# Kernel tuning notes

Measured on AMD Instinct MI355X. Metric: run time of the kernel, lower is better.

The kernel has to match this reference:

```python
import jax, jax.numpy as jnp
import numpy as np

DIM = 2048
NH = 16
Q_LORA = 1536
KV_LORA = 512
NOPE = 128
ROPE = 64
VDIM = 128
QK = NOPE + ROPE  # 192
B, S = 2, 2048
EPS = 1.1920929e-07  # torch.finfo(float32).eps (nn.RMSNorm default)


def linear(x, w, b):
    return jnp.einsum('...i,oi->...o', x, w) + b


def rmsnorm(x, w):
    ms = jnp.mean(x * x, axis=-1, keepdims=True)
    return x * jax.lax.rsqrt(ms + EPS) * w


def rope(x, cos, sin):
    # x: [B,S,H,d] interleaved pairs; cos/sin: [S, d//2]
    x = x.reshape(*x.shape[:-1], -1, 2)
    x0, x1 = x[..., 0], x[..., 1]
    c = cos[None, :, None, :]
    s = sin[None, :, None, :]
    y0 = x0 * c - x1 * s
    y1 = x0 * s + x1 * c
    return jnp.stack([y0, y1], axis=-1).reshape(*x.shape[:-2], -1)


def setup_inputs() -> dict:
    key = jax.random.key(0)
    ks = jax.random.split(key, 12)
    sd = 0.02
    x = jax.random.normal(ks[0], (B, S, DIM), dtype=jnp.float32)
    freqs = jax.random.normal(ks[1], (S, ROPE // 2), dtype=jnp.float32)
    causal_mask = jnp.where(jnp.triu(jnp.ones((S, S), bool), k=1), -1e9, 0.0).astype(jnp.float32)
    inp = dict(x=x, freqs=freqs, causal_mask=causal_mask)
    inp['Wq_down_w'] = sd * jax.random.normal(ks[2], (Q_LORA, DIM), dtype=jnp.float32)
    inp['Wq_down_b'] = jnp.zeros((Q_LORA,), jnp.float32)
    inp['q_norm_w'] = jnp.ones((Q_LORA,), jnp.float32)
    inp['Wq_up_w'] = sd * jax.random.normal(ks[3], (NH * QK, Q_LORA), dtype=jnp.float32)
    inp['Wq_up_b'] = jnp.zeros((NH * QK,), jnp.float32)
    inp['Wkv_down_w'] = sd * jax.random.normal(ks[4], (KV_LORA + ROPE, DIM), dtype=jnp.float32)
    inp['Wkv_down_b'] = jnp.zeros((KV_LORA + ROPE,), jnp.float32)
    inp['kv_norm_w'] = jnp.ones((KV_LORA,), jnp.float32)
    inp['Wkv_up_w'] = sd * jax.random.normal(ks[5], (NH * (NOPE + VDIM), KV_LORA), dtype=jnp.float32)
    inp['Wkv_up_b'] = jnp.zeros((NH * (NOPE + VDIM),), jnp.float32)
    inp['Wo_w'] = sd * jax.random.normal(ks[6], (DIM, NH * VDIM), dtype=jnp.float32)
    inp['Wo_b'] = jnp.zeros((DIM,), jnp.float32)
    return inp


def reference(x, freqs, causal_mask, Wq_down_w, Wq_down_b, q_norm_w, Wq_up_w, Wq_up_b,
              Wkv_down_w, Wkv_down_b, kv_norm_w, Wkv_up_w, Wkv_up_b, Wo_w, Wo_b):
    cos, sin = jnp.cos(freqs), jnp.sin(freqs)
    scale = QK ** -0.5
    # Q path: low-rank down, RMSNorm, up
    q_lat = rmsnorm(linear(x, Wq_down_w, Wq_down_b), q_norm_w)
    Q = linear(q_lat, Wq_up_w, Wq_up_b).reshape(B, S, NH, QK)
    Q_nope, Q_rope = Q[..., :NOPE], Q[..., NOPE:]
    Q_rope = rope(Q_rope, cos, sin)
    Q = jnp.concatenate([Q_nope, Q_rope], axis=-1)  # [B,S,H,QK]
    # KV path: shared latent + decoupled rope key
    kv_kr = linear(x, Wkv_down_w, Wkv_down_b)
    kv_lat, K_rope = kv_kr[..., :KV_LORA], kv_kr[..., KV_LORA:]
    kv_lat = rmsnorm(kv_lat, kv_norm_w)
    K_rope = rope(K_rope[:, :, None, :], cos, sin)  # [B,S,1,ROPE]
    kv = linear(kv_lat, Wkv_up_w, Wkv_up_b).reshape(B, S, NH, NOPE + VDIM)
    K_nope, V = kv[..., :NOPE], kv[..., NOPE:]
    K = jnp.concatenate([K_nope, jnp.broadcast_to(K_rope, (B, S, NH, ROPE))], axis=-1)
    # attention
    scores = jnp.einsum('bqhd,bkhd->bhqk', Q, K) * scale + causal_mask[None, None]
    attn = jax.nn.softmax(scores, axis=-1)
    out = jnp.einsum('bhqk,bkhd->bqhd', attn, V).reshape(B, S, NH * VDIM)
    return linear(out, Wo_w, Wo_b)
```

## Files before the change

kernel.cpp:

```cpp
#include <hip/hip_runtime.h>
#include <hip/hip_bf16.h>

#define DIMD 2048
#define NHD 16
#define QLORA 1536
#define KVLORA 512
#define QKD 192
#define BBD 2
#define SSD 2048
#define BSD (BBD*SSD)
#define KVPAD 640
#define BHN (BBD*NHD)
#define EPSF 1.1920929e-07f
#define SCALEF 0.07216878364870322f

typedef __hip_bfloat16 bf16;
typedef __attribute__((ext_vector_type(8))) short short8;
typedef __attribute__((ext_vector_type(4))) float floatx4;

typedef __attribute__((address_space(1))) char as1_char;
typedef __attribute__((address_space(3))) char as3_char;
#define GLD16(g, l) __builtin_amdgcn_global_load_lds((as1_char*)(g), (as3_char*)(l), 16, 0, 0)

__device__ __forceinline__ float block_sum(float x) {
#pragma unroll
  for (int o = 32; o > 0; o >>= 1) x += __shfl_xor(x, o, 64);
  __shared__ float red[4];
  __syncthreads();
  if ((threadIdx.x & 63) == 0) red[threadIdx.x >> 6] = x;
  __syncthreads();
  return red[0] + red[1] + red[2] + red[3];
}

template<bool STORE_BF16>
__global__ __launch_bounds__(256)
void gemm_bt(const bf16* __restrict__ A, const bf16* __restrict__ Bm,
             const float* __restrict__ bias, void* __restrict__ Cp,
             int M, int N, int K, long sA, long sB, long sC, int ldc)
{
  int m0 = blockIdx.y * 128, n0 = blockIdx.x * 128;
  long z = blockIdx.z;
  A  += z * sA;
  Bm += z * sB;

  __shared__ __align__(16) bf16 Asm[128 * 32];
  __shared__ __align__(16) bf16 Bsm[128 * 32];

  const int tid  = threadIdx.x;
  const int lane = tid & 63;
  const int wv   = tid >> 6;
  const int wm   = (wv >> 1) << 6;
  const int wn   = (wv & 1) << 6;
  const int fr   = lane & 15;
  const int q8   = (lane >> 4) << 3;

  floatx4 acc[4][4];
#pragma unroll
  for (int i = 0; i < 4; ++i)
#pragma unroll
    for (int j = 0; j < 4; ++j)
      acc[i][j] = (floatx4){0.f, 0.f, 0.f, 0.f};

  for (int k0 = 0; k0 < K; k0 += 32) {
    __syncthreads();
#pragma unroll
    for (int it = 0; it < 2; ++it) {
      int seg = it * 256 + tid;
      int row = seg >> 2, cs = seg & 3;
      GLD16(A  + (long)(m0 + row) * K + k0 + cs * 8, &Asm[(it * 256 + wv * 64) * 8]);
      GLD16(Bm + (long)(n0 + row) * K + k0 + cs * 8, &Bsm[(it * 256 + wv * 64) * 8]);
    }
    __syncthreads();

    short8 fa[4], fb[4];
#pragma unroll
    for (int t = 0; t < 4; ++t) fa[t] = *(const short8*)&Asm[(wm + t * 16 + fr) * 32 + q8];
#pragma unroll
    for (int t = 0; t < 4; ++t) fb[t] = *(const short8*)&Bsm[(wn + t * 16 + fr) * 32 + q8];
#pragma unroll
    for (int i = 0; i < 4; ++i)
#pragma unroll
      for (int j = 0; j < 4; ++j)
        acc[i][j] = __builtin_amdgcn_mfma_f32_16x16x32_bf16(fa[i], fb[j], acc[i][j], 0, 0, 0);
  }

  long cb = z * sC;
  int rq = (lane >> 4) * 4;
#pragma unroll
  for (int i = 0; i < 4; ++i) {
#pragma unroll
    for (int j = 0; j < 4; ++j) {
      int col = n0 + wn + j * 16 + fr;
      float bv = bias ? bias[col] : 0.f;
#pragma unroll
      for (int r = 0; r < 4; ++r) {
        int rowg = m0 + wm + i * 16 + rq + r;
        float v = acc[i][j][r] + bv;
        if (STORE_BF16)
          ((bf16*)Cp)[cb + (long)rowg * ldc + col] = __float2bfloat16(v);
        else
          ((float*)Cp)[cb + (long)rowg * ldc + col] = v;
      }
    }
  }
}

__global__ __launch_bounds__(512, 2)
void flash_attn(const bf16* __restrict__ Qh, const bf16* __restrict__ Kh,
                const bf16* __restrict__ Vt, bf16* __restrict__ attnall)
{
  const int p = blockIdx.y;
  const int z = blockIdx.x;
  const int b = z >> 4, h = z & 15;

  const bf16* Qg = Qh + (long)z * SSD * QKD;
  const bf16* Kg = Kh + (long)z * SSD * QKD;
  const bf16* Vg = Vt + (long)z * 128 * SSD;

  __shared__ __align__(16) bf16 KB[3][6 * 2048];
  __shared__ __align__(16) bf16 VB[3][2 * 4096];
  __shared__ __align__(16) bf16 PB[2 * 4096];

  const int tid  = threadIdx.x;
  const int lane = tid & 63;
  const int wv   = tid >> 6;
  const int fr   = lane & 15;
  const int g4   = lane >> 4;

  long kofs[3]; int kdst[3];
#pragma unroll
  for (int it = 0; it < 3; ++it) {
    int gseg = it * 512 + tid;
    int c = gseg >> 8, rs = gseg & 255;
    int r = rs >> 2, s = (rs & 3) ^ ((r >> 1) & 3);
    kofs[it] = (long)r * QKD + c * 32 + s * 8;
    kdst[it] = c * 2048 + rs * 8;
  }
  long vofs[2]; int vdst[2];
#pragma unroll
  for (int it = 0; it < 2; ++it) {
    int gseg = it * 512 + tid;
    int c2 = gseg >> 9, ds = gseg & 511;
    int d = ds >> 2, s = (ds & 3) ^ ((d >> 1) & 3);
    vofs[it] = (long)d * SSD + c2 * 32 + s * 8;
    vdst[it] = c2 * 4096 + ds * 8;
  }
  const int qrow = wv * 16 + fr;
  const int prow_off = qrow * 32 + (((g4 ^ (qrow >> 1)) & 3) << 3);
  int fsw[4];
#pragma unroll
  for (int n = 0; n < 4; ++n) {
    int row = n * 16 + fr;
    fsw[n] = row * 32 + (((g4 ^ (row >> 1)) & 3) << 3);
  }
  int vsw[8];
#pragma unroll
  for (int dn = 0; dn < 8; ++dn) {
    int row = dn * 16 + fr;
    vsw[dn] = row * 32 + (((g4 ^ (row >> 1)) & 3) << 3);
  }
  const int qr = tid >> 2;
  const int qs = (tid & 3) ^ ((qr >> 1) & 3);

  auto stageKV = [&](int jb2, bf16* kb2, bf16* vb2) {
#pragma unroll
    for (int it = 0; it < 3; ++it)
      GLD16(Kg + (long)jb2 * QKD + kofs[it], kb2 + kdst[it]);
#pragma unroll
    for (int it = 0; it < 2; ++it)
      GLD16(Vg + jb2 + vofs[it], vb2 + vdst[it]);
  };

#pragma unroll 1
  for (int t = 0; t < 2; ++t) {
    const int qt = t ? p : 15 - p;
    const int q0 = qt << 7;
    const int jmax = 2 * qt + 1;

    __syncthreads();
#pragma unroll
    for (int c = 0; c < 6; ++c)
      GLD16(Qg + (long)(q0 + qr) * QKD + c * 32 + qs * 8, &KB[0][0] + c * 4096 + tid * 8);
    __syncthreads();
    short8 qf[6];
#pragma unroll
    for (int c = 0; c < 6; ++c)
      qf[c] = *(const short8*)(&KB[0][0] + c * 4096 + prow_off);
    __syncthreads();

    floatx4 oacc[8];
#pragma unroll
    for (int n = 0; n < 8; ++n) oacc[n] = (floatx4){0.f, 0.f, 0.f, 0.f};
    float mi[4], li[4];
#pragma unroll
    for (int r = 0; r < 4; ++r) { mi[r] = -1e30f; li[r] = 0.f; }

    stageKV(0, &KB[0][0], &VB[0][0]);
    if (jmax >= 1) stageKV(64, &KB[1][0], &VB[1][0]);

#pragma unroll 1
    for (int j = 0; j <= jmax; ++j) {
      const int jb = j << 6;
      if (j + 2 <= jmax) {
        const int bi = (j + 2) % 3;
        stageKV((j + 2) << 6, &KB[bi][0], &VB[bi][0]);
        asm volatile("s_waitcnt vmcnt(10)" ::: "memory");
      } else if (j + 1 <= jmax) {
        asm volatile("s_waitcnt vmcnt(5)" ::: "memory");
      } else {
        asm volatile("s_waitcnt vmcnt(0)" ::: "memory");
      }
      __builtin_amdgcn_sched_barrier(0);
      __builtin_amdgcn_s_barrier();
      __builtin_amdgcn_sched_barrier(0);

      const bf16* kb = &KB[j % 3][0];
      const bf16* vb = &VB[j % 3][0];
      const bool active = (jb <= q0 + wv * 16 + 15);
      if (active) {
        floatx4 sacc[4];
#pragma unroll
        for (int n = 0; n < 4; ++n) sacc[n] = (floatx4){0.f, 0.f, 0.f, 0.f};
        __builtin_amdgcn_s_setprio(1);
#pragma unroll
        for (int c = 0; c < 6; ++c) {
#pragma unroll
          for (int n = 0; n < 4; ++n) {
            short8 fb = *(const short8*)(kb + c * 2048 + fsw[n]);
            sacc[n] = __builtin_amdgcn_mfma_f32_16x16x32_bf16(qf[c], fb, sacc[n], 0, 0, 0);
          }
        }
        __builtin_amdgcn_s_setprio(0);

        const bool diag = (jb + 63 > q0 + wv * 16);
#pragma unroll
        for (int r = 0; r < 4; ++r) {
          int rowg = q0 + wv * 16 + g4 * 4 + r;
          float mx = -1e30f;
#pragma unroll
          for (int n = 0; n < 4; ++n) {
            float v = sacc[n][r] * SCALEF;
            if (diag && (jb + n * 16 + fr) > rowg) v = -1e30f;
            sacc[n][r] = v;
            mx = fmaxf(mx, v);
          }
#pragma unroll
          for (int off = 1; off < 16; off <<= 1) mx = fmaxf(mx, __shfl_xor(mx, off, 64));
          float mnew = fmaxf(mi[r], mx);
          float alpha = __expf(mi[r] - mnew);
          mi[r] = mnew;
          float rs = 0.f;
#pragma unroll
          for (int n = 0; n < 4; ++n) {
            float pv = __expf(sacc[n][r] - mnew);
            sacc[n][r] = pv;
            rs += pv;
          }
#pragma unroll
          for (int off = 1; off < 16; off <<= 1) rs += __shfl_xor(rs, off, 64);
          li[r] = li[r] * alpha + rs;
#pragma unroll
          for (int n = 0; n < 8; ++n) oacc[n][r] *= alpha;
        }

#pragma unroll
        for (int n = 0; n < 4; ++n) {
          int c2 = n >> 1;
          int col = (n & 1) * 16 + fr;
#pragma unroll
          for (int r = 0; r < 4; ++r) {
            int m = wv * 16 + g4 * 4 + r;
            int cw = (((col >> 3) ^ ((m >> 1) & 3)) << 3) | (col & 7);
            PB[c2 * 4096 + m * 32 + cw] = __float2bfloat16(sacc[n][r]);
          }
        }

        __builtin_amdgcn_s_setprio(1);
#pragma unroll
        for (int c2 = 0; c2 < 2; ++c2) {
          short8 pf = *(const short8*)&PB[c2 * 4096 + prow_off];
#pragma unroll
          for (int dn = 0; dn < 8; ++dn) {
            short8 vf = *(const short8*)(vb + c2 * 4096 + vsw[dn]);
            oacc[dn] = __builtin_amdgcn_mfma_f32_16x16x32_bf16(pf, vf, oacc[dn], 0, 0, 0);
          }
        }
        __builtin_amdgcn_s_setprio(0);
      }
      __builtin_amdgcn_sched_barrier(0);
      __builtin_amdgcn_s_barrier();
      __builtin_amdgcn_sched_barrier(0);
    }

#pragma unroll
    for (int r = 0; r < 4; ++r) {
      float inv = 1.f / li[r];
      int m = q0 + wv * 16 + g4 * 4 + r;
      bf16* orow = attnall + ((long)(b * SSD + m) * NHD + h) * 128;
#pragma unroll
      for (int dn = 0; dn < 8; ++dn)
        orow[dn * 16 + fr] = __float2bfloat16(oacc[dn][r] * inv);
    }
  }
}

__device__ __forceinline__ void cvt4(const float* __restrict__ s, bf16* __restrict__ d,
                                     long se, long de) {
  float4 v = *(const float4*)(s + se);
  union { bf16 h[4]; uint2 u; } o;
  o.h[0] = __float2bfloat16(v.x); o.h[1] = __float2bfloat16(v.y);
  o.h[2] = __float2bfloat16(v.z); o.h[3] = __float2bfloat16(v.w);
  *(uint2*)(d + de) = o.u;
}

#define NX4   ((long)BSD * DIMD / 4)
#define NQD4  ((long)QLORA * DIMD / 4)
#define NQU4  ((long)3072 * QLORA / 4)
#define NKVD4 ((long)KVPAD * DIMD / 4)
#define NKVU4 ((long)4096 * KVLORA / 4)
#define NWO4  ((long)DIMD * 2048 / 4)

__global__ __launch_bounds__(256)
void cvt_all(const float* __restrict__ x, const float* __restrict__ wqd,
             const float* __restrict__ wqu, const float* __restrict__ wkvd,
             const float* __restrict__ wkvu, const float* __restrict__ wo,
             bf16* __restrict__ dx, bf16* __restrict__ dwqd, bf16* __restrict__ dwqu,
             bf16* __restrict__ dwkvd, bf16* __restrict__ dwkvu, bf16* __restrict__ dwo)
{
  long i = (long)blockIdx.x * 256 + threadIdx.x;
  if (i < NX4) { cvt4(x, dx, i * 4, i * 4); return; }
  i -= NX4;
  if (i < NQD4) { cvt4(wqd, dwqd, i * 4, i * 4); return; }
  i -= NQD4;
  if (i < NQU4) { cvt4(wqu, dwqu, i * 4, i * 4); return; }
  i -= NQU4;
  if (i < NKVD4) {
    long e = i * 4;
    long r = e >> 11;
    if (r < 576) cvt4(wkvd, dwkvd, e, e);
    else *(uint2*)(dwkvd + e) = (uint2){0u, 0u};
    return;
  }
  i -= NKVD4;
  if (i < NKVU4) { cvt4(wkvu, dwkvu, i * 4, i * 4); return; }
  i -= NKVU4;
  if (i < NWO4) { cvt4(wo, dwo, i * 4, i * 4); return; }
}

template<int L>
__global__ __launch_bounds__(256)
void rmsnorm_k(const bf16* __restrict__ in, const float* __restrict__ bias,
               const float* __restrict__ w, bf16* __restrict__ out, int ldin)
{
  constexpr int NIT = L / 256;
  long r = blockIdx.x;
  const bf16* row = in + r * ldin;
  int tid = threadIdx.x;
  float v[NIT];
  float ss = 0.f;
#pragma unroll
  for (int i = 0; i < NIT; ++i) {
    int c = tid + (i << 8);
    float x = __bfloat162float(row[c]) + (bias ? bias[c] : 0.f);
    v[i] = x;
    ss += x * x;
  }
  ss = block_sum(ss);
  float sc = rsqrtf(ss / (float)L + EPSF);
#pragma unroll
  for (int i = 0; i < NIT; ++i) {
    int c = tid + (i << 8);
    out[r * L + c] = __float2bfloat16(v[i] * sc * w[c]);
  }
}

__global__ void build_q(const bf16* __restrict__ Qf, const float* __restrict__ freqs,
                        bf16* __restrict__ Qh)
{
  int idx = blockIdx.x * 256 + threadIdx.x;
  if (idx >= BSD * NHD * 96) return;
  int j = idx % 96;
  int h = (idx / 96) % NHD;
  int srow = idx / (96 * NHD);
  int s = srow & (SSD - 1);
  int b = srow >> 11;
  const bf16* src = Qf + (long)srow * (NHD * QKD) + h * QKD + 2 * j;
  float x0 = __bfloat162float(src[0]), x1 = __bfloat162float(src[1]), y0, y1;
  if (j >= 64) {
    int i = j - 64;
    float f = freqs[s * 32 + i];
    float c = cosf(f), sn = sinf(f);
    y0 = x0 * c - x1 * sn;
    y1 = x0 * sn + x1 * c;
  } else { y0 = x0; y1 = x1; }
  bf16* dst = Qh + ((long)(b * NHD + h) * SSD + s) * QKD + 2 * j;
  dst[0] = __float2bfloat16(y0);
  dst[1] = __float2bfloat16(y1);
}

__global__ void build_k(const bf16* __restrict__ kvf, const bf16* __restrict__ kvkr,
                        const float* __restrict__ kvb, const float* __restrict__ freqs,
                        bf16* __restrict__ Kh)
{
  int idx = blockIdx.x * 256 + threadIdx.x;
  if (idx >= BSD * NHD * 96) return;
  int j = idx % 96;
  int h = (idx / 96) % NHD;
  int srow = idx / (96 * NHD);
  int s = srow & (SSD - 1);
  int b = srow >> 11;
  float y0, y1;
  if (j < 64) {
    const bf16* src = kvf + (long)srow * 4096 + h * 256 + 2 * j;
    y0 = __bfloat162float(src[0]); y1 = __bfloat162float(src[1]);
  } else {
    int i = j - 64;
    float x0 = __bfloat162float(kvkr[(long)srow * KVPAD + 512 + 2 * i]) + kvb[512 + 2 * i];
    float x1 = __bfloat162float(kvkr[(long)srow * KVPAD + 513 + 2 * i]) + kvb[513 + 2 * i];
    float f = freqs[s * 32 + i];
    float c = cosf(f), sn = sinf(f);
    y0 = x0 * c - x1 * sn;
    y1 = x0 * sn + x1 * c;
  }
  bf16* dst = Kh + ((long)(b * NHD + h) * SSD + s) * QKD + 2 * j;
  dst[0] = __float2bfloat16(y0);
  dst[1] = __float2bfloat16(y1);
}

__global__ __launch_bounds__(256)
void build_vt(const bf16* __restrict__ kvf, bf16* __restrict__ Vt)
{
  __shared__ float t[32][33];
  int s0 = blockIdx.x * 32, d0 = blockIdx.y * 32, z = blockIdx.z;
  int b = z / NHD, h = z % NHD;
  int tx = threadIdx.x, ty = threadIdx.y;
#pragma unroll
  for (int r = 0; r < 4; ++r) {
    int sl = ty + r * 8;
    t[sl][tx] = __bfloat162float(kvf[(long)(b * SSD + s0 + sl) * 4096 + h * 256 + 128 + d0 + tx]);
  }
  __syncthreads();
#pragma unroll
  for (int r = 0; r < 4; ++r) {
    int dl = ty + r * 8;
    Vt[((long)z * 128 + d0 + dl) * SSD + s0 + tx] = __float2bfloat16(t[tx][dl]);
  }
}

__global__ void diag_fill(float* out) { out[blockIdx.x * 256 + threadIdx.x] = 1000.0f; }

extern "C" void kernel_launch(void* const* d_in, const int* in_sizes, int n_in,
                              void* d_out, int out_size, void* d_ws, size_t ws_size,
                              hipStream_t stream)
{
  const float* x     = (const float*)d_in[0];
  const float* freqs = (const float*)d_in[1];
  const float* Wqd   = (const float*)d_in[3];
  const float* Wqdb  = (const float*)d_in[4];
  const float* qnw   = (const float*)d_in[5];
  const float* Wqu   = (const float*)d_in[6];
  const float* Wqub  = (const float*)d_in[7];
  const float* Wkvd  = (const float*)d_in[8];
  const float* Wkvdb = (const float*)d_in[9];
  const float* kvnw  = (const float*)d_in[10];
  const float* Wkvu  = (const float*)d_in[11];
  const float* Wkvub = (const float*)d_in[12];
  const float* Wo    = (const float*)d_in[13];
  const float* Wob   = (const float*)d_in[14];
  float* out = (float*)d_out;

  char* ws = (char*)d_ws;
  size_t off = 0;
  auto alloc = [&](size_t bytes) {
    void* p = ws + off;
    off += (bytes + 255) & ~(size_t)255;
    return p;
  };

  bf16* Wqd16  = (bf16*)alloc((size_t)QLORA * DIMD * 2);
  bf16* Wqu16  = (bf16*)alloc((size_t)3072 * QLORA * 2);
  bf16* Wkvd16 = (bf16*)alloc((size_t)KVPAD * DIMD * 2);
  bf16* Wkvu16 = (bf16*)alloc((size_t)4096 * KVLORA * 2);
  bf16* Wo16   = (bf16*)alloc((size_t)DIMD * 2048 * 2);
  bf16* x16    = (bf16*)alloc((size_t)BSD * DIMD * 2);
  bf16* Ra     = (bf16*)alloc((size_t)BSD * QLORA * 2);
  bf16* Rb     = (bf16*)alloc((size_t)BSD * QLORA * 2);
  bf16* Rc     = (bf16*)alloc((size_t)BSD * 4096 * 2);
  bf16* Qh16   = (bf16*)alloc((size_t)BHN * SSD * QKD * 2);
  bf16* Kh16   = (bf16*)alloc((size_t)BHN * SSD * QKD * 2);
  bf16* Vt16   = (bf16*)alloc((size_t)BHN * 128 * SSD * 2);

  bf16* qdown   = Ra;  bf16* kvkr    = Ra;
  bf16* qlat16  = Rb;  bf16* kvlat16 = Rb;
  bf16* Qf      = Rc;  bf16* kvf     = Rc;  bf16* attnall = Rc;

  if (off > ws_size) { diag_fill<<<8, 256, 0, stream>>>(out); return; }

  dim3 blk(256);
  auto cdiv = [](long a, long b) { return (int)((a + b - 1) / b); };

  long tot4 = NX4 + NQD4 + NQU4 + NKVD4 + NKVU4 + NWO4;
  cvt_all<<<cdiv(tot4, 256), blk, 0, stream>>>(x, Wqd, Wqu, Wkvd, Wkvu, Wo,
                                               x16, Wqd16, Wqu16, Wkvd16, Wkvu16, Wo16);

  gemm_bt<true><<<dim3(QLORA / 128, BSD / 128, 1), blk, 0, stream>>>(
      x16, Wqd16, Wqdb, qdown, BSD, QLORA, DIMD, 0, 0, 0, QLORA);
  rmsnorm_k<QLORA><<<BSD, blk, 0, stream>>>(qdown, nullptr, qnw, qlat16, QLORA);
  gemm_bt<true><<<dim3(3072 / 128, BSD / 128, 1), blk, 0, stream>>>(
      qlat16, Wqu16, Wqub, Qf, BSD, 3072, QLORA, 0, 0, 0, 3072);
  build_q<<<cdiv((long)BSD * NHD * 96, 256), blk, 0, stream>>>(Qf, freqs, Qh16);

  gemm_bt<true><<<dim3(KVPAD / 128, BSD / 128, 1), blk, 0, stream>>>(
      x16, Wkvd16, nullptr, kvkr, BSD, KVPAD, DIMD, 0, 0, 0, KVPAD);
  rmsnorm_k<KVLORA><<<BSD, blk, 0, stream>>>(kvkr, Wkvdb, kvnw, kvlat16, KVPAD);
  gemm_bt<true><<<dim3(4096 / 128, BSD / 128, 1), blk, 0, stream>>>(
      kvlat16, Wkvu16, Wkvub, kvf, BSD, 4096, KVLORA, 0, 0, 0, 4096);
  build_k<<<cdiv((long)BSD * NHD * 96, 256), blk, 0, stream>>>(kvf, kvkr, Wkvdb, freqs, Kh16);
  build_vt<<<dim3(SSD / 32, 128 / 32, BHN), dim3(32, 8), 0, stream>>>(kvf, Vt16);

  flash_attn<<<dim3(BHN, 8), dim3(512), 0, stream>>>(Qh16, Kh16, Vt16, attnall);

  gemm_bt<false><<<dim3(2048 / 128, BSD / 128, 1), blk, 0, stream>>>(
      attnall, Wo16, Wob, out, BSD, DIMD, 2048, 0, 0, 0, DIMD);
}
```

Measured before the change: 567.2 us.

## Restructure flash attention to 4 waves with 32 rows each; remap GEMM tiles per XCD

Flash attention now launches one 256-thread block per (batch-head, query tile) over 512 blocks instead of 512-thread blocks that each handled two tiles. Each wave processes 32 query rows, so every K and V fragment read from LDS feeds two MFMAs. The kernel double-buffers K/V instead of triple-buffering and writes P into the spent K buffer, which saves LDS but adds an extra barrier per iteration. The softmax scale is folded into Q during build_q, sincos uses the fast intrinsic, and the GEMM remaps workgroups so adjacent tiles land on the same XCD for better L2 reuse.

```diff
diff --git a/kernel.cpp b/kernel.cpp
--- a/kernel.cpp
+++ b/kernel.cpp
@@ -38,7 +38,14 @@
              const float* __restrict__ bias, void* __restrict__ Cp,
              int M, int N, int K, long sA, long sB, long sC, int ldc)
 {
-  int m0 = blockIdx.y * 128, n0 = blockIdx.x * 128;
+  int nwg = gridDim.x * gridDim.y;
+  int lin = blockIdx.y * gridDim.x + blockIdx.x;
+  int xcd = lin & 7, l8 = lin >> 3;
+  int qd = nwg >> 3, rd = nwg & 7;
+  int wg = (xcd < rd ? xcd * (qd + 1) : rd * (qd + 1) + (xcd - rd) * qd) + l8;
+  int bx = wg % gridDim.x, by = wg / gridDim.x;
+
+  int m0 = by * 128, n0 = bx * 128;
   long z = blockIdx.z;
   A  += z * sA;
   Bm += z * sB;
@@ -105,21 +112,22 @@
   }
 }
 
-__global__ __launch_bounds__(512, 2)
+__global__ __launch_bounds__(256, 2)
 void flash_attn(const bf16* __restrict__ Qh, const bf16* __restrict__ Kh,
                 const bf16* __restrict__ Vt, bf16* __restrict__ attnall)
 {
-  const int p = blockIdx.y;
-  const int z = blockIdx.x;
-  const int b = z >> 4, h = z & 15;
-
-  const bf16* Qg = Qh + (long)z * SSD * QKD;
-  const bf16* Kg = Kh + (long)z * SSD * QKD;
-  const bf16* Vg = Vt + (long)z * 128 * SSD;
-
-  __shared__ __align__(16) bf16 KB[3][6 * 2048];
-  __shared__ __align__(16) bf16 VB[3][2 * 4096];
-  __shared__ __align__(16) bf16 PB[2 * 4096];
+  const int lin = blockIdx.x;
+  const int bh  = lin & 31;
+  const int g   = lin >> 5;
+  const int qt  = (g < 8) ? (15 - g) : (g - 8);
+  const int b = bh >> 4, h = bh & 15;
+
+  const bf16* Qg = Qh + (long)bh * SSD * QKD;
+  const bf16* Kg = Kh + (long)bh * SSD * QKD;
+  const bf16* Vg = Vt + (long)bh * 128 * SSD;
+
+  __shared__ __align__(16) bf16 KB[2][12288];
+  __shared__ __align__(16) bf16 VB[2][8192];
 
   const int tid  = threadIdx.x;
   const int lane = tid & 63;
@@ -127,26 +135,15 @@
   const int fr   = lane & 15;
   const int g4   = lane >> 4;
 
-  long kofs[3]; int kdst[3];
-#pragma unroll
-  for (int it = 0; it < 3; ++it) {
-    int gseg = it * 512 + tid;
-    int c = gseg >> 8, rs = gseg & 255;
-    int r = rs >> 2, s = (rs & 3) ^ ((r >> 1) & 3);
-    kofs[it] = (long)r * QKD + c * 32 + s * 8;
-    kdst[it] = c * 2048 + rs * 8;
-  }
-  long vofs[2]; int vdst[2];
-#pragma unroll
-  for (int it = 0; it < 2; ++it) {
-    int gseg = it * 512 + tid;
-    int c2 = gseg >> 9, ds = gseg & 511;
-    int d = ds >> 2, s = (ds & 3) ^ ((d >> 1) & 3);
-    vofs[it] = (long)d * SSD + c2 * 32 + s * 8;
-    vdst[it] = c2 * 4096 + ds * 8;
-  }
-  const int qrow = wv * 16 + fr;
-  const int prow_off = qrow * 32 + (((g4 ^ (qrow >> 1)) & 3) << 3);
+  const int kr = tid >> 2;
+  const int ks = (tid & 3) ^ ((kr >> 1) & 3);
+  int dv[2], sv[2];
+#pragma unroll
+  for (int par = 0; par < 2; ++par) {
+    int rs = par * 256 + tid;
+    dv[par] = rs >> 2;
+    sv[par] = (rs & 3) ^ ((dv[par] >> 1) & 3);
+  }
   int fsw[4];
 #pragma unroll
   for (int n = 0; n < 4; ++n) {
@@ -159,147 +156,180 @@
     int row = dn * 16 + fr;
     vsw[dn] = row * 32 + (((g4 ^ (row >> 1)) & 3) << 3);
   }
-  const int qr = tid >> 2;
-  const int qs = (tid & 3) ^ ((qr >> 1) & 3);
+  int qoff[2];
+#pragma unroll
+  for (int i = 0; i < 2; ++i) {
+    int row = wv * 32 + i * 16 + fr;
+    qoff[i] = row * 32 + (((g4 ^ (row >> 1)) & 3) << 3);
+  }
+
+  const int q0   = qt << 7;
+  const int jmax = 2 * qt + 1;
 
   auto stageKV = [&](int jb2, bf16* kb2, bf16* vb2) {
 #pragma unroll
-    for (int it = 0; it < 3; ++it)
-      GLD16(Kg + (long)jb2 * QKD + kofs[it], kb2 + kdst[it]);
-#pragma unroll
-    for (int it = 0; it < 2; ++it)
-      GLD16(Vg + jb2 + vofs[it], vb2 + vdst[it]);
+    for (int c = 0; c < 6; ++c)
+      GLD16(Kg + (long)(jb2 + kr) * QKD + c * 32 + ks * 8, kb2 + c * 2048 + tid * 8);
+#pragma unroll
+    for (int it = 0; it < 4; ++it) {
+      int c2 = it >> 1, par = it & 1;
+      GLD16(Vg + (long)dv[par] * SSD + jb2 + c2 * 32 + sv[par] * 8,
+            vb2 + c2 * 4096 + (par * 256 + tid) * 8);
+    }
   };
 
+#pragma unroll
+  for (int it = 0; it < 12; ++it) {
+    int c = it >> 1, par = it & 1;
+    GLD16(Qg + (long)(q0 + dv[par]) * QKD + c * 32 + sv[par] * 8,
+          &KB[0][0] + c * 4096 + (par * 256 + tid) * 8);
+  }
+  __syncthreads();
+  short8 qf[2][6];
+#pragma unroll
+  for (int i = 0; i < 2; ++i)
+#pragma unroll
+    for (int c = 0; c < 6; ++c)
+      qf[i][c] = *(const short8*)(&KB[0][0] + c * 4096 + qoff[i]);
+
+  floatx4 oacc[2][8];
+#pragma unroll
+  for (int i = 0; i < 2; ++i)
+#pragma unroll
+    for (int n = 0; n < 8; ++n) oacc[i][n] = (floatx4){0.f, 0.f, 0.f, 0.f};
+  float mi[2][4], li[2][4];
+#pragma unroll
+  for (int i = 0; i < 2; ++i)
+#pragma unroll
+    for (int r = 0; r < 4; ++r) { mi[i][r] = -1e30f; li[i][r] = 0.f; }
+
+  __syncthreads();
+
+  stageKV(0, &KB[0][0], &VB[0][0]);
+
 #pragma unroll 1
-  for (int t = 0; t < 2; ++t) {
-    const int qt = t ? p : 15 - p;
-    const int q0 = qt << 7;
-    const int jmax = 2 * qt + 1;
-
-    __syncthreads();
-#pragma unroll
-    for (int c = 0; c < 6; ++c)
-      GLD16(Qg + (long)(q0 + qr) * QKD + c * 32 + qs * 8, &KB[0][0] + c * 4096 + tid * 8);
-    __syncthreads();
-    short8 qf[6];
-#pragma unroll
-    for (int c = 0; c < 6; ++c)
-      qf[c] = *(const short8*)(&KB[0][0] + c * 4096 + prow_off);
-    __syncthreads();
-
-    floatx4 oacc[8];
-#pragma unroll
-    for (int n = 0; n < 8; ++n) oacc[n] = (floatx4){0.f, 0.f, 0.f, 0.f};
-    float mi[4], li[4];
-#pragma unroll
-    for (int r = 0; r < 4; ++r) { mi[r] = -1e30f; li[r] = 0.f; }
-
-    stageKV(0, &KB[0][0], &VB[0][0]);
-    if (jmax >= 1) stageKV(64, &KB[1][0], &VB[1][0]);
-
-#pragma unroll 1
-    for (int j = 0; j <= jmax; ++j) {
-      const int jb = j << 6;
-      if (j + 2 <= jmax) {
-        const int bi = (j + 2) % 3;
-        stageKV((j + 2) << 6, &KB[bi][0], &VB[bi][0]);
-        asm volatile("s_waitcnt vmcnt(10)" ::: "memory");
-      } else if (j + 1 <= jmax) {
-        asm volatile("s_waitcnt vmcnt(5)" ::: "memory");
-      } else {
-        asm volatile("s_waitcnt vmcnt(0)" ::: "memory");
+  for (int j = 0; j <= jmax; ++j) {
+    const int jb = j << 6;
+    if (j < jmax) {
+      stageKV((j + 1) << 6, &KB[(j + 1) & 1][0], &VB[(j + 1) & 1][0]);
+      asm volatile("s_waitcnt vmcnt(10)" ::: "memory");
+    } else {
+      asm volatile("s_waitcnt vmcnt(0)" ::: "memory");
+    }
+    __builtin_amdgcn_sched_barrier(0);
+    __builtin_amdgcn_s_barrier();
+    __builtin_amdgcn_sched_barrier(0);
+
+    bf16* kb = &KB[j & 1][0];
+    const bf16* vb = &VB[j & 1][0];
+    const bool active = (jb <= q0 + wv * 32 + 31);
+    floatx4 sacc[2][4];
+    if (active) {
+#pragma unroll
+      for (int i = 0; i < 2; ++i)
+#pragma unroll
+        for (int n = 0; n < 4; ++n) sacc[i][n] = (floatx4){0.f, 0.f, 0.f, 0.f};
+      __builtin_amdgcn_s_setprio(1);
+#pragma unroll
+      for (int c = 0; c < 6; ++c) {
+#pragma unroll
+        for (int n = 0; n < 4; ++n) {
+          short8 fb = *(const short8*)(kb + c * 2048 + fsw[n]);
+#pragma unroll
+          for (int i = 0; i < 2; ++i)
+            sacc[i][n] = __builtin_amdgcn_mfma_f32_16x16x32_bf16(qf[i][c], fb, sacc[i][n], 0, 0, 0);
+        }
       }
-      __builtin_amdgcn_sched_barrier(0);
-      __builtin_amdgcn_s_barrier();
-      __builtin_amdgcn_sched_barrier(0);
-
-      const bf16* kb = &KB[j % 3][0];
-      const bf16* vb = &VB[j % 3][0];
-      const bool active = (jb <= q0 + wv * 16 + 15);
-      if (active) {
-        floatx4 sacc[4];
-#pragma unroll
-        for (int n = 0; n < 4; ++n) sacc[n] = (floatx4){0.f, 0.f, 0.f, 0.f};
-        __builtin_amdgcn_s_setprio(1);
-#pragma unroll
-        for (int c = 0; c < 6; ++c) {
+      __builtin_amdgcn_s_setprio(0);
+
+#pragma unroll
+      for (int i = 0; i < 2; ++i) {
+        const bool diag = (jb + 63 > q0 + wv * 32 + i * 16);
+#pragma unroll
+        for (int r = 0; r < 4; ++r) {
+          int rowg = q0 + wv * 32 + i * 16 + g4 * 4 + r;
+          if (diag) {
+#pragma unroll
+            for (int n = 0; n < 4; ++n)
+              if ((jb + n * 16 + fr) > rowg) sacc[i][n][r] = -1e30f;
+          }
+          float mx = fmaxf(fmaxf(sacc[i][0][r], sacc[i][1][r]),
+                           fmaxf(sacc[i][2][r], sacc[i][3][r]));
+#pragma unroll
+          for (int off = 1; off < 16; off <<= 1) mx = fmaxf(mx, __shfl_xor(mx, off, 64));
+          float mnew = fmaxf(mi[i][r], mx);
+          float alpha = __expf(mi[i][r] - mnew);
+          mi[i][r] = mnew;
+          float rs = 0.f;
 #pragma unroll
           for (int n = 0; n < 4; ++n) {
-            short8 fb = *(const short8*)(kb + c * 2048 + fsw[n]);
-            sacc[n] = __builtin_amdgcn_mfma_f32_16x16x32_bf16(qf[c], fb, sacc[n], 0, 0, 0);
-          }
-        }
-        __builtin_amdgcn_s_setprio(0);
-
-        const bool diag = (jb + 63 > q0 + wv * 16);
-#pragma unroll
-        for (int r = 0; r < 4; ++r) {
-          int rowg = q0 + wv * 16 + g4 * 4 + r;
-          float mx = -1e30f;
-#pragma unroll
-          for (int n = 0; n < 4; ++n) {
-            float v = sacc[n][r] * SCALEF;
-            if (diag && (jb + n * 16 + fr) > rowg) v = -1e30f;
-            sacc[n][r] = v;
-            mx = fmaxf(mx, v);
-          }
-#pragma unroll
-          for (int off = 1; off < 16; off <<= 1) mx = fmaxf(mx, __shfl_xor(mx, off, 64));
-          float mnew = fmaxf(mi[r], mx);
-          float alpha = __expf(mi[r] - mnew);
-          mi[r] = mnew;
-          float rs = 0.f;
-#pragma unroll
-          for (int n = 0; n < 4; ++n) {
-            float pv = __expf(sacc[n][r] - mnew);
-            sacc[n][r] = pv;
+            float pv = __expf(sacc[i][n][r] - mnew);
+            sacc[i][n][r] = pv;
             rs += pv;
           }
 #pragma unroll
           for (int off = 1; off < 16; off <<= 1) rs += __shfl_xor(rs, off, 64);
-          li[r] = li[r] * alpha + rs;
-#pragma unroll
-          for (int n = 0; n < 8; ++n) oacc[n][r] *= alpha;
+          li[i][r] = li[i][r] * alpha + rs;
+#pragma unroll
+          for (int n = 0; n < 8; ++n) oacc[i][n][r] *= alpha;
         }
-
+      }
+    }
+
+    __builtin_amdgcn_sched_barrier(0);
+    __builtin_amdgcn_s_barrier();
+    __builtin_amdgcn_sched_barrier(0);
+
+    if (active) {
+      bf16* pb = kb;
+#pragma unroll
+      for (int i = 0; i < 2; ++i) {
 #pragma unroll
         for (int n = 0; n < 4; ++n) {
           int c2 = n >> 1;
           int col = (n & 1) * 16 + fr;
 #pragma unroll
           for (int r = 0; r < 4; ++r) {
-            int m = wv * 16 + g4 * 4 + r;
+            int m = wv * 32 + i * 16 + g4 * 4 + r;
             int cw = (((col >> 3) ^ ((m >> 1) & 3)) << 3) | (col & 7);
-            PB[c2 * 4096 + m * 32 + cw] = __float2bfloat16(sacc[n][r]);
+            pb[c2 * 4096 + m * 32 + cw] = __float2bfloat16(sacc[i][n][r]);
           }
         }
-
-        __builtin_amdgcn_s_setprio(1);
-#pragma unroll
-        for (int c2 = 0; c2 < 2; ++c2) {
-          short8 pf = *(const short8*)&PB[c2 * 4096 + prow_off];
-#pragma unroll
-          for (int dn = 0; dn < 8; ++dn) {
-            short8 vf = *(const short8*)(vb + c2 * 4096 + vsw[dn]);
-            oacc[dn] = __builtin_amdgcn_mfma_f32_16x16x32_bf16(pf, vf, oacc[dn], 0, 0, 0);
-          }
+      }
+
+      __builtin_amdgcn_s_setprio(1);
+#pragma unroll
+      for (int c2 = 0; c2 < 2; ++c2) {
+        short8 pf[2];
+#pragma unroll
+        for (int i = 0; i < 2; ++i)
+          pf[i] = *(const short8*)(pb + c2 * 4096 + qoff[i]);
+#pragma unroll
+        for (int dn = 0; dn < 8; ++dn) {
+          short8 vf = *(const short8*)(vb + c2 * 4096 + vsw[dn]);
+#pragma unroll
+          for (int i = 0; i < 2; ++i)
+            oacc[i][dn] = __builtin_amdgcn_mfma_f32_16x16x32_bf16(pf[i], vf, oacc[i][dn], 0, 0, 0);
         }
-        __builtin_amdgcn_s_setprio(0);
       }
-      __builtin_amdgcn_sched_barrier(0);
-      __builtin_amdgcn_s_barrier();
-      __builtin_amdgcn_sched_barrier(0);
-    }
-
+      __builtin_amdgcn_s_setprio(0);
+    }
+
+    __builtin_amdgcn_sched_barrier(0);
+    __builtin_amdgcn_s_barrier();
+    __builtin_amdgcn_sched_barrier(0);
+  }
+
+#pragma unroll
+  for (int i = 0; i < 2; ++i) {
 #pragma unroll
     for (int r = 0; r < 4; ++r) {
-      float inv = 1.f / li[r];
-      int m = q0 + wv * 16 + g4 * 4 + r;
+      float inv = 1.f / li[i][r];
+      int m = q0 + wv * 32 + i * 16 + g4 * 4 + r;
       bf16* orow = attnall + ((long)(b * SSD + m) * NHD + h) * 128;
 #pragma unroll
       for (int dn = 0; dn < 8; ++dn)
-        orow[dn * 16 + fr] = __float2bfloat16(oacc[dn][r] * inv);
+        orow[dn * 16 + fr] = __float2bfloat16(oacc[i][dn][r] * inv);
     }
   }
 }
@@ -389,13 +419,14 @@
   if (j >= 64) {
     int i = j - 64;
     float f = freqs[s * 32 + i];
-    float c = cosf(f), sn = sinf(f);
+    float c, sn;
+    __sincosf(f, &sn, &c);
     y0 = x0 * c - x1 * sn;
     y1 = x0 * sn + x1 * c;
   } else { y0 = x0; y1 = x1; }
   bf16* dst = Qh + ((long)(b * NHD + h) * SSD + s) * QKD + 2 * j;
-  dst[0] = __float2bfloat16(y0);
-  dst[1] = __float2bfloat16(y1);
+  dst[0] = __float2bfloat16(y0 * SCALEF);
+  dst[1] = __float2bfloat16(y1 * SCALEF);
 }
 
 __global__ void build_k(const bf16* __restrict__ kvf, const bf16* __restrict__ kvkr,
@@ -418,7 +449,8 @@
     float x0 = __bfloat162float(kvkr[(long)srow * KVPAD + 512 + 2 * i]) + kvb[512 + 2 * i];
     float x1 = __bfloat162float(kvkr[(long)srow * KVPAD + 513 + 2 * i]) + kvb[513 + 2 * i];
     float f = freqs[s * 32 + i];
-    float c = cosf(f), sn = sinf(f);
+    float c, sn;
+    __sincosf(f, &sn, &c);
     y0 = x0 * c - x1 * sn;
     y1 = x0 * sn + x1 * c;
   }
@@ -518,7 +550,7 @@
   build_k<<<cdiv((long)BSD * NHD * 96, 256), blk, 0, stream>>>(kvf, kvkr, Wkvdb, freqs, Kh16);
   build_vt<<<dim3(SSD / 32, 128 / 32, BHN), dim3(32, 8), 0, stream>>>(kvf, Vt16);
 
-  flash_attn<<<dim3(BHN, 8), dim3(512), 0, stream>>>(Qh16, Kh16, Vt16, attnall);
+  flash_attn<<<dim3(512), blk, 0, stream>>>(Qh16, Kh16, Vt16, attnall);
 
   gemm_bt<false><<<dim3(2048 / 128, BSD / 128, 1), blk, 0, stream>>>(
       attnall, Wo16, Wob, out, BSD, DIMD, 2048, 0, 0, 0, DIMD);
```

New measurement: 609.8 us. 7.5% more time.
